# Performance work log

Measured on AMD Instinct MI355X. Metric: run time of the kernel, lower is better.

Reference implementation:

```python
import jax, jax.numpy as jnp
import numpy as np

ALPHA = 0.2        # LeakyReLU negative slope
MASK_VAL = -9e15   # matches torch -9000000000000000.0


def setup_inputs() -> dict:
    key = jax.random.key(0)
    k_h, k_adj, k_w, k_a = jax.random.split(key, 4)
    B, N, Nodes, IF, OF = 8, 8, 512, 256, 256
    h = jax.random.normal(k_h, (B, N, Nodes, IF), dtype=jnp.float32)
    adj = jax.random.randint(k_adj, (Nodes, Nodes), 0, 2, dtype=jnp.int32)
    # xavier_uniform with gain=1.414
    gain = 1.414
    lim_w = gain * np.sqrt(6.0 / (IF + OF))
    W = jax.random.uniform(k_w, (IF, OF), dtype=jnp.float32, minval=-lim_w, maxval=lim_w)
    lim_a = gain * np.sqrt(6.0 / (2 * OF + 1))
    a = jax.random.uniform(k_a, (2 * OF, 1), dtype=jnp.float32, minval=-lim_a, maxval=lim_a)
    return {"h": h, "adj": adj, "W": W, "a": a}


def reference(h, adj, W, a):
    # Wh: [B, N, Nodes, OF]
    Wh = jnp.matmul(h, W)
    OF = W.shape[1]
    a1, a2 = a[:OF, 0], a[OF:, 0]
    # e[..., i, j] = leakyrelu(a1 . Wh_i + a2 . Wh_j)  (decomposed additive attention)
    src = jnp.einsum('bnif,f->bni', Wh, a1)  # [B, N, Nodes]
    dst = jnp.einsum('bnjf,f->bnj', Wh, a2)  # [B, N, Nodes]
    e = jax.nn.leaky_relu(src[..., :, None] + dst[..., None, :], negative_slope=ALPHA)
    attention = jnp.where(adj > 0, e, jnp.full_like(e, MASK_VAL))
    attention = jax.nn.softmax(attention, axis=-1)
    # dropout is identity in eval mode (training=False)
    h_prime = jnp.matmul(attention, Wh)  # [B, N, Nodes, OF]
    return jax.nn.elu(h_prime)  # concat=True
```

## Files before the change

### kernel.cpp

```cpp
#include <hip/hip_runtime.h>
#include <hip/hip_bf16.h>


#define ALPHA 0.2f
#define MASK_VAL -9000000000000000.0f
#define NODES 512
#define FDIM 256
#define BN 64

typedef float  f32x4 __attribute__((ext_vector_type(4)));
typedef int    i32x4 __attribute__((ext_vector_type(4)));
typedef short  s16x8 __attribute__((ext_vector_type(8)));
typedef short  s16x4 __attribute__((ext_vector_type(4)));
typedef __bf16 bf16x8 __attribute__((ext_vector_type(8)));

__device__ __forceinline__ unsigned short f2bfu(float x) {
    __hip_bfloat16 b = __float2bfloat16(x);
    unsigned short u; __builtin_memcpy(&u, &b, 2); return u;
}
__device__ __forceinline__ float bfu2f(unsigned short u) {
    unsigned int w = ((unsigned int)u) << 16; return __uint_as_float(w);
}
__device__ __forceinline__ f32x4 mfma16(s16x8 a, s16x8 b, f32x4 c) {
    return __builtin_amdgcn_mfma_f32_16x16x32_bf16(
        __builtin_bit_cast(bf16x8, a), __builtin_bit_cast(bf16x8, b), c, 0, 0, 0);
}

__device__ __forceinline__ void split8v(f32x4 v0, f32x4 v1, s16x8& hi, s16x8& lo)
{
    float x[8] = {v0[0], v0[1], v0[2], v0[3], v1[0], v1[1], v1[2], v1[3]};
    unsigned hw[4], lw[4];
    #pragma unroll
    for (int d = 0; d < 4; ++d) {
        const unsigned u0 = __float_as_uint(x[2*d]);
        const unsigned u1 = __float_as_uint(x[2*d + 1]);
        hw[d] = __builtin_amdgcn_perm(u1, u0, 0x07060302);
        const float l0 = x[2*d]     - __uint_as_float(u0 & 0xFFFF0000u);
        const float l1 = x[2*d + 1] - __uint_as_float(u1 & 0xFFFF0000u);
        lw[d] = __builtin_amdgcn_perm(__float_as_uint(l1), __float_as_uint(l0),
                                      0x07060302);
    }
    hi = __builtin_bit_cast(s16x8, *(unsigned(*)[4])hw);
    lo = __builtin_bit_cast(s16x8, *(unsigned(*)[4])lw);
}

__device__ __forceinline__ void gll16(const void* g, void* l) {
    __builtin_amdgcn_global_load_lds(
        (const __attribute__((address_space(1))) unsigned int*)g,
        (__attribute__((address_space(3))) unsigned int*)l,
        16, 0, 0);
}

__global__ __launch_bounds__(256) void detect_kernel(const unsigned short* __restrict__ hraw,
                                                     int* __restrict__ flag)
{
    const int tid = threadIdx.x;
    float m = 0.0f;
    for (int i = tid; i < 16384; i += 256) {
        unsigned int w = ((unsigned int)hraw[i]) << 16;
        float v = __uint_as_float(w);
        v = fabsf(v);
        if (!(v == v)) v = 1e30f;
        m = fmaxf(m, v);
    }
    #pragma unroll
    for (int off = 32; off >= 1; off >>= 1)
        m = fmaxf(m, __shfl_down(m, off));
    __shared__ float red[4];
    if ((tid & 63) == 0) red[tid >> 6] = m;
    __syncthreads();
    if (tid == 0) {
        float mm = fmaxf(fmaxf(red[0], red[1]), fmaxf(red[2], red[3]));
        *flag = (mm > 1e4f) ? 1 : 0;
    }
}

__global__ __launch_bounds__(256) void prep_w_kernel(
    const void* __restrict__ Wv, const int* __restrict__ flagp,
    short* __restrict__ WtHi, short* __restrict__ WtLo)
{
    const int flag = *flagp;
    __shared__ float tile[16][17];
    const int tx = threadIdx.x & 15, ty = threadIdx.x >> 4;
    const int kk = blockIdx.y * 16 + ty;
    const int f  = blockIdx.x * 16 + tx;
    float v;
    if (flag) v = ((const float*)Wv)[kk * FDIM + f];
    else      v = bfu2f(((const unsigned short*)Wv)[kk * FDIM + f]);
    tile[ty][tx] = v;
    __syncthreads();
    const float x = tile[tx][ty];
    const int fo = blockIdx.x * 16 + ty;
    const int ko = blockIdx.y * 16 + tx;
    unsigned short h = f2bfu(x);
    WtHi[fo * FDIM + ko] = (short)h;
    WtLo[fo * FDIM + ko] = (short)f2bfu(x - bfu2f(h));
}

__global__ __launch_bounds__(256, 2) void wh_gemm(
    const void* __restrict__ hv,
    const short* __restrict__ WtHi, const short* __restrict__ WtLo,
    const void* __restrict__ av, const int* __restrict__ flagp,
    short* __restrict__ WhTHi, short* __restrict__ WhTLo,
    float* __restrict__ srcv, float* __restrict__ dstv)
{
    __shared__ __align__(16) char smem[81920];
    char* As = smem;
    char* Bh = smem + 16384;
    char* Bl = smem + 49152;

    const int flag = *flagp;
    const int blk = blockIdx.x;
    const int bn  = blk >> 3;
    const int i0  = (blk & 7) * 64;
    const size_t r0g = (size_t)blk * 64;
    const int tid = threadIdx.x;
    const int w = tid >> 6, l = tid & 63;
    const int fb = l & 15, g = l >> 4;
    const unsigned wub = (unsigned)(tid & ~63);

    f32x4 acc[4][4];
    #pragma unroll
    for (int rt = 0; rt < 4; ++rt)
        #pragma unroll
        for (int ct = 0; ct < 4; ++ct) acc[rt][ct] = f32x4{0.f,0.f,0.f,0.f};

    auto stageBhl = [&](int buf, int k0) {
        #pragma unroll
        for (int i = 0; i < 4; ++i) {
            const int idx = i * 256 + tid;
            const int f = idx >> 2, sg = idx & 3;
            const int ss = sg ^ ((f ^ (f >> 2)) & 3);
            char* d = (char*)(size_t)((i * 256 + (int)wub) * 16);
            gll16(WtHi + f * FDIM + k0 + ss * 8, Bh + buf * 16384 + (size_t)d);
            gll16(WtLo + f * FDIM + k0 + ss * 8, Bl + buf * 16384 + (size_t)d);
        }
    };
    auto stageBh = [&](int buf, int k0) {
        #pragma unroll
        for (int i = 0; i < 4; ++i) {
            const int idx = i * 256 + tid;
            const int f = idx >> 2, sg = idx & 3;
            const int ss = sg ^ ((f ^ (f >> 2)) & 3);
            gll16(WtHi + f * FDIM + k0 + ss * 8,
                  Bh + buf * 16384 + (i * 256 + (int)wub) * 16);
        }
    };
    auto stageAf = [&](int buf, int k0) {
        #pragma unroll
        for (int i = 0; i < 2; ++i) {
            const int idx = i * 256 + tid;
            const int row = idx >> 3, sg = idx & 7;
            const int ss = sg ^ (row & 7);
            gll16((const float*)hv + (r0g + row) * FDIM + k0 + ss * 4,
                  As + buf * 8192 + (i * 256 + (int)wub) * 16);
        }
    };
    auto stageAb = [&](int buf, int k0) {
        const int row = tid >> 2, sg = tid & 3;
        const int ss = sg ^ ((row >> 1) & 3);
        gll16((const short*)hv + (r0g + row) * FDIM + k0 + ss * 8,
              As + buf * 4096 + (int)wub * 16);
    };

    if (flag) {
        stageAf(0, 0); stageBhl(0, 0);
        __syncthreads();
        for (int t = 0; t < 8; ++t) {
            const int cur = t & 1, nxt = cur ^ 1;
            if (t < 7) { stageAf(nxt, (t + 1) * 32); stageBhl(nxt, (t + 1) * 32); }
            s16x8 bhf[4], blf[4];
            #pragma unroll
            for (int ct = 0; ct < 4; ++ct) {
                const int f = w * 64 + ct * 16 + fb;
                const int slot = g ^ ((f ^ (f >> 2)) & 3);
                const unsigned off = (unsigned)(cur * 16384 + f * 64 + slot * 16);
                bhf[ct] = *(const s16x8*)(Bh + off);
                blf[ct] = *(const s16x8*)(Bl + off);
            }
            #pragma unroll
            for (int rt = 0; rt < 4; ++rt) {
                const int row = rt * 16 + fb;
                const int s0 = (2 * g) ^ (row & 7), s1 = (2 * g + 1) ^ (row & 7);
                const f32x4 v0 = *(const f32x4*)(As + cur * 8192 + row * 128 + s0 * 16);
                const f32x4 v1 = *(const f32x4*)(As + cur * 8192 + row * 128 + s1 * 16);
                s16x8 ah, al; split8v(v0, v1, ah, al);
                #pragma unroll
                for (int ct = 0; ct < 4; ++ct) {
                    acc[rt][ct] = mfma16(ah, bhf[ct], acc[rt][ct]);
                    acc[rt][ct] = mfma16(al, bhf[ct], acc[rt][ct]);
                    acc[rt][ct] = mfma16(ah, blf[ct], acc[rt][ct]);
                }
            }
            __syncthreads();
        }
    } else {
        stageAb(0, 0); stageBh(0, 0);
        __syncthreads();
        for (int t = 0; t < 8; ++t) {
            const int cur = t & 1, nxt = cur ^ 1;
            if (t < 7) { stageAb(nxt, (t + 1) * 32); stageBh(nxt, (t + 1) * 32); }
            s16x8 bhf[4];
            #pragma unroll
            for (int ct = 0; ct < 4; ++ct) {
                const int f = w * 64 + ct * 16 + fb;
                const int slot = g ^ ((f ^ (f >> 2)) & 3);
                bhf[ct] = *(const s16x8*)(Bh + cur * 16384 + f * 64 + slot * 16);
            }
            #pragma unroll
            for (int rt = 0; rt < 4; ++rt) {
                const int row = rt * 16 + fb;
                const int slot = g ^ ((row >> 1) & 3);
                const s16x8 a = *(const s16x8*)(As + cur * 4096 + row * 64 + slot * 16);
                #pragma unroll
                for (int ct = 0; ct < 4; ++ct)
                    acc[rt][ct] = mfma16(a, bhf[ct], acc[rt][ct]);
            }
            __syncthreads();
        }
    }

    const size_t wbT = (size_t)bn * FDIM * NODES;
    #pragma unroll
    for (int rt = 0; rt < 4; ++rt) {
        const int orow = i0 + rt * 16 + g * 4;
        #pragma unroll
        for (int ct = 0; ct < 4; ++ct) {
            const int f = w * 64 + ct * 16 + fb;
            s16x4 h4, l4;
            #pragma unroll
            for (int r = 0; r < 4; ++r) {
                float x = acc[rt][ct][r];
                unsigned short hh = f2bfu(x);
                h4[r] = (short)hh;
                l4[r] = (short)f2bfu(x - bfu2f(hh));
            }
            *(s16x4*)(WhTHi + wbT + (size_t)f * NODES + orow) = h4;
            *(s16x4*)(WhTLo + wbT + (size_t)f * NODES + orow) = l4;
        }
    }

    float a1v[4], a2v[4];
    #pragma unroll
    for (int ct = 0; ct < 4; ++ct) {
        const int f = w * 64 + ct * 16 + fb;
        if (flag) {
            a1v[ct] = ((const float*)av)[f];
            a2v[ct] = ((const float*)av)[FDIM + f];
        } else {
            a1v[ct] = bfu2f(((const unsigned short*)av)[f]);
            a2v[ct] = bfu2f(((const unsigned short*)av)[FDIM + f]);
        }
    }
    float* red1 = (float*)smem;
    float* red2 = red1 + 256;
    #pragma unroll
    for (int rt = 0; rt < 4; ++rt) {
        #pragma unroll
        for (int r = 0; r < 4; ++r) {
            float s1 = 0.f, s2 = 0.f;
            #pragma unroll
            for (int ct = 0; ct < 4; ++ct) {
                s1 = fmaf(acc[rt][ct][r], a1v[ct], s1);
                s2 = fmaf(acc[rt][ct][r], a2v[ct], s2);
            }
            #pragma unroll
            for (int off = 1; off <= 8; off <<= 1) {
                s1 += __shfl_xor(s1, off);
                s2 += __shfl_xor(s2, off);
            }
            if (fb == 0) {
                red1[w * 64 + rt * 16 + g * 4 + r] = s1;
                red2[w * 64 + rt * 16 + g * 4 + r] = s2;
            }
        }
    }
    __syncthreads();
    if (tid < 64) {
        srcv[bn * NODES + i0 + tid] =
            red1[tid] + red1[64 + tid] + red1[128 + tid] + red1[192 + tid];
        dstv[bn * NODES + i0 + tid] =
            red2[tid] + red2[64 + tid] + red2[128 + tid] + red2[192 + tid];
    }
}

__global__ __launch_bounds__(512, 2) void pv_gemm(
    const short* __restrict__ WhTHi, const short* __restrict__ WhTLo,
    const float* __restrict__ srcv, const float* __restrict__ dstv,
    const int* __restrict__ adj, const int* __restrict__ flagp,
    void* __restrict__ out)
{
    __shared__ __align__(16) char smem[131328];
    char* Ps = smem;
    char* Bh = smem + 65536;
    char* Bl = smem + 98304;
    float* rowinvS = (float*)(smem + 131072);

    const int flag = *flagp;
    const int b0 = blockIdx.x;
    const int blk = (b0 & 7) * 64 + (b0 >> 3);
    const int bn  = blk >> 3;
    const int i0  = (blk & 7) * 64;
    const int tid = threadIdx.x;
    const int w = tid >> 6, l = tid & 63;
    const unsigned wub = (unsigned)(tid & ~63);

    const short* bhig = WhTHi + (size_t)bn * FDIM * NODES;
    const short* blog = WhTLo + (size_t)bn * FDIM * NODES;

    auto stageB = [&](int buf, int k0) {
        #pragma unroll
        for (int i = 0; i < 2; ++i) {
            const int idx = i * 512 + tid;
            const int f = idx >> 2, sg = idx & 3;
            const int ss = sg ^ ((f ^ (f >> 2)) & 3);
            const int d = (i * 512 + (int)wub) * 16;
            gll16(bhig + (size_t)f * NODES + k0 + ss * 8, Bh + buf * 16384 + d);
            gll16(blog + (size_t)f * NODES + k0 + ss * 8, Bl + buf * 16384 + d);
        }
    };

    stageB(0, 0);

    {
        const float* drow = dstv + bn * NODES;
        const int j = l * 8;
        for (int rr = 0; rr < 8; ++rr) {
            const int r = w * 8 + rr;
            const int* adjrow = adj + (size_t)(i0 + r) * NODES;
            const float srow = srcv[bn * NODES + i0 + r];
            const i32x4 q0 = *(const i32x4*)(adjrow + j);
            const i32x4 q1 = *(const i32x4*)(adjrow + j + 4);
            const f32x4 d0 = *(const f32x4*)(drow + j);
            const f32x4 d1 = *(const f32x4*)(drow + j + 4);
            float e[8];
            #pragma unroll
            for (int k = 0; k < 4; ++k) {
                float ev = srow + d0[k];
                ev = (ev > 0.f) ? ev : ALPHA * ev;
                e[k] = (q0[k] > 0) ? ev : MASK_VAL;
                float ew = srow + d1[k];
                ew = (ew > 0.f) ? ew : ALPHA * ew;
                e[4 + k] = (q1[k] > 0) ? ew : MASK_VAL;
            }
            float m = e[0];
            #pragma unroll
            for (int k = 1; k < 8; ++k) m = fmaxf(m, e[k]);
            #pragma unroll
            for (int off = 1; off <= 32; off <<= 1) m = fmaxf(m, __shfl_xor(m, off));
            float s = 0.f;
            s16x8 ph;
            #pragma unroll
            for (int k = 0; k < 8; ++k) {
                float p = __expf(e[k] - m);
                s += p;
                ph[k] = (short)f2bfu(p);
            }
            #pragma unroll
            for (int off = 1; off <= 32; off <<= 1) s += __shfl_xor(s, off);
            *(s16x8*)(Ps + r * 1024 + ((l ^ (r & 7)) * 16)) = ph;
            if (l == 0) rowinvS[r] = 1.0f / s;
        }
    }
    __syncthreads();

    const int fb = l & 15, g = l >> 4;
    const int wr = w >> 2, wc = w & 3;

    f32x4 acc[2][4];
    #pragma unroll
    for (int rt = 0; rt < 2; ++rt)
        #pragma unroll
        for (int ct = 0; ct < 4; ++ct) acc[rt][ct] = f32x4{0.f,0.f,0.f,0.f};

    for (int t = 0; t < 16; ++t) {
        const int cur = t & 1, nxt = cur ^ 1;
        if (t < 15) stageB(nxt, (t + 1) * 32);
        s16x8 bhf[4], blf[4];
        #pragma unroll
        for (int ct = 0; ct < 4; ++ct) {
            const int f = wc * 64 + ct * 16 + fb;
            const int slot = g ^ ((f ^ (f >> 2)) & 3);
            const unsigned off = (unsigned)(cur * 16384 + f * 64 + slot * 16);
            bhf[ct] = *(const s16x8*)(Bh + off);
            blf[ct] = *(const s16x8*)(Bl + off);
        }
        s16x8 af[2];
        #pragma unroll
        for (int rt = 0; rt < 2; ++rt) {
            const int row = wr * 32 + rt * 16 + fb;
            const int seg = 4 * t + g;
            af[rt] = *(const s16x8*)(Ps + row * 1024 + ((seg ^ (row & 7)) * 16));
        }
        #pragma unroll
        for (int rt = 0; rt < 2; ++rt)
            #pragma unroll
            for (int ct = 0; ct < 4; ++ct) {
                acc[rt][ct] = mfma16(af[rt], bhf[ct], acc[rt][ct]);
                acc[rt][ct] = mfma16(af[rt], blf[ct], acc[rt][ct]);
            }
        __syncthreads();
    }

    #pragma unroll
    for (int rt = 0; rt < 2; ++rt) {
        const int rbase = wr * 32 + rt * 16 + g * 4;
        float inv[4];
        #pragma unroll
        for (int r = 0; r < 4; ++r) inv[r] = rowinvS[rbase + r];
        #pragma unroll
        for (int ct = 0; ct < 4; ++ct) {
            const int f = wc * 64 + ct * 16 + fb;
            #pragma unroll
            for (int r = 0; r < 4; ++r) {
                float v = acc[rt][ct][r] * inv[r];
                v = (v > 0.f) ? v : expm1f(v);
                const size_t o = ((size_t)bn * NODES + i0 + rbase + r) * FDIM + f;
                if (flag) ((float*)out)[o] = v;
                else      ((unsigned short*)out)[o] = f2bfu(v);
            }
        }
    }
}

extern "C" void kernel_launch(void* const* d_in, const int* in_sizes, int n_in,
                              void* d_out, int out_size, void* d_ws, size_t ws_size,
                              hipStream_t stream)
{
    const void* h   = d_in[0];
    const int*  adj = (const int*)d_in[1];
    const void* W   = d_in[2];
    const void* a   = d_in[3];

    int*   flag  = (int*)d_ws;
    float* srcv  = (float*)d_ws + 64;
    float* dstv  = srcv + BN * NODES;
    short* WtHi  = (short*)(dstv + BN * NODES);
    short* WtLo  = WtHi + FDIM * FDIM;
    short* WhTHi = WtLo + FDIM * FDIM;
    short* WhTLo = WhTHi + (size_t)BN * FDIM * NODES;

    detect_kernel<<<1, 256, 0, stream>>>((const unsigned short*)h, flag);
    prep_w_kernel<<<dim3(16, 16), 256, 0, stream>>>(W, flag, WtHi, WtLo);
    wh_gemm<<<512, 256, 0, stream>>>(h, WtHi, WtLo, a, flag,
                                     WhTHi, WhTLo, srcv, dstv);
    pv_gemm<<<512, 512, 0, stream>>>(WhTHi, WhTLo, srcv, dstv, adj, flag, d_out);
}
```

Measured before the change: 174.7 us.

## Restructure GAT GEMM pipelines: register-split A staging, triple-buffered PV with 1024 threads

Measured after the change: 164.1 us. -6.1%, faster.

```diff
diff --git a/kernel.cpp b/kernel.cpp
--- a/kernel.cpp
+++ b/kernel.cpp
@@ -105,9 +105,6 @@
     float* __restrict__ srcv, float* __restrict__ dstv)
 {
     __shared__ __align__(16) char smem[81920];
-    char* As = smem;
-    char* Bh = smem + 16384;
-    char* Bl = smem + 49152;
 
     const int flag = *flagp;
     const int blk = blockIdx.x;
@@ -117,7 +114,25 @@
     const int tid = threadIdx.x;
     const int w = tid >> 6, l = tid & 63;
     const int fb = l & 15, g = l >> 4;
-    const unsigned wub = (unsigned)(tid & ~63);
+
+    const int arow = tid >> 2, asg = tid & 3;
+    const int aseg = asg ^ ((arow >> 1) & 3);
+    const int awr  = arow * 64 + asg * 16;
+
+    const short* gBh[4];
+    const short* gBl[4];
+    int bdst[4];
+    {
+        const int bsg = tid & 3;
+        #pragma unroll
+        for (int i = 0; i < 4; ++i) {
+            const int f = i * 64 + (tid >> 2);
+            const int ss = bsg ^ ((f ^ (f >> 2)) & 3);
+            gBh[i] = WtHi + f * FDIM + ss * 8;
+            gBl[i] = WtLo + f * FDIM + ss * 8;
+            bdst[i] = (i * 256 + tid) * 16;
+        }
+    }
 
     f32x4 acc[4][4];
     #pragma unroll
@@ -125,97 +140,106 @@
         #pragma unroll
         for (int ct = 0; ct < 4; ++ct) acc[rt][ct] = f32x4{0.f,0.f,0.f,0.f};
 
-    auto stageBhl = [&](int buf, int k0) {
-        #pragma unroll
-        for (int i = 0; i < 4; ++i) {
-            const int idx = i * 256 + tid;
-            const int f = idx >> 2, sg = idx & 3;
-            const int ss = sg ^ ((f ^ (f >> 2)) & 3);
-            char* d = (char*)(size_t)((i * 256 + (int)wub) * 16);
-            gll16(WtHi + f * FDIM + k0 + ss * 8, Bh + buf * 16384 + (size_t)d);
-            gll16(WtLo + f * FDIM + k0 + ss * 8, Bl + buf * 16384 + (size_t)d);
-        }
-    };
-    auto stageBh = [&](int buf, int k0) {
-        #pragma unroll
-        for (int i = 0; i < 4; ++i) {
-            const int idx = i * 256 + tid;
-            const int f = idx >> 2, sg = idx & 3;
-            const int ss = sg ^ ((f ^ (f >> 2)) & 3);
-            gll16(WtHi + f * FDIM + k0 + ss * 8,
-                  Bh + buf * 16384 + (i * 256 + (int)wub) * 16);
-        }
-    };
-    auto stageAf = [&](int buf, int k0) {
-        #pragma unroll
-        for (int i = 0; i < 2; ++i) {
-            const int idx = i * 256 + tid;
-            const int row = idx >> 3, sg = idx & 7;
-            const int ss = sg ^ (row & 7);
-            gll16((const float*)hv + (r0g + row) * FDIM + k0 + ss * 4,
-                  As + buf * 8192 + (i * 256 + (int)wub) * 16);
-        }
-    };
-    auto stageAb = [&](int buf, int k0) {
-        const int row = tid >> 2, sg = tid & 3;
-        const int ss = sg ^ ((row >> 1) & 3);
-        gll16((const short*)hv + (r0g + row) * FDIM + k0 + ss * 8,
-              As + buf * 4096 + (int)wub * 16);
-    };
-
     if (flag) {
-        stageAf(0, 0); stageBhl(0, 0);
+        const float* gA = (const float*)hv + (r0g + arow) * FDIM + aseg * 8;
+        {
+            f32x4 v0 = *(const f32x4*)gA;
+            f32x4 v1 = *(const f32x4*)(gA + 4);
+            #pragma unroll
+            for (int i = 0; i < 4; ++i) {
+                gll16(gBh[i], smem + 16384 + bdst[i]);
+                gll16(gBl[i], smem + 49152 + bdst[i]);
+            }
+            s16x8 hi, lo; split8v(v0, v1, hi, lo);
+            *(s16x8*)(smem + awr) = hi;
+            *(s16x8*)(smem + 4096 + awr) = lo;
+        }
         __syncthreads();
         for (int t = 0; t < 8; ++t) {
             const int cur = t & 1, nxt = cur ^ 1;
-            if (t < 7) { stageAf(nxt, (t + 1) * 32); stageBhl(nxt, (t + 1) * 32); }
-            s16x8 bhf[4], blf[4];
+            f32x4 v0 = {}, v1 = {};
+            if (t < 7) {
+                v0 = *(const f32x4*)(gA + (t+1)*32);
+                v1 = *(const f32x4*)(gA + (t+1)*32 + 4);
+                #pragma unroll
+                for (int i = 0; i < 4; ++i) {
+                    gll16(gBh[i] + (t+1)*32, smem + 16384 + nxt*16384 + bdst[i]);
+                    gll16(gBl[i] + (t+1)*32, smem + 49152 + nxt*16384 + bdst[i]);
+                }
+            }
+            s16x8 bh[4], bl[4], ah[4], al[4];
             #pragma unroll
             for (int ct = 0; ct < 4; ++ct) {
-                const int f = w * 64 + ct * 16 + fb;
+                const int f = w*64 + ct*16 + fb;
                 const int slot = g ^ ((f ^ (f >> 2)) & 3);
-                const unsigned off = (unsigned)(cur * 16384 + f * 64 + slot * 16);
-                bhf[ct] = *(const s16x8*)(Bh + off);
-                blf[ct] = *(const s16x8*)(Bl + off);
+                const int off = 16384 + cur*16384 + f*64 + slot*16;
+                bh[ct] = *(const s16x8*)(smem + off);
+                bl[ct] = *(const s16x8*)(smem + off + 32768);
             }
             #pragma unroll
             for (int rt = 0; rt < 4; ++rt) {
-                const int row = rt * 16 + fb;
-                const int s0 = (2 * g) ^ (row & 7), s1 = (2 * g + 1) ^ (row & 7);
-                const f32x4 v0 = *(const f32x4*)(As + cur * 8192 + row * 128 + s0 * 16);
-                const f32x4 v1 = *(const f32x4*)(As + cur * 8192 + row * 128 + s1 * 16);
-                s16x8 ah, al; split8v(v0, v1, ah, al);
+                const int row = rt*16 + fb;
+                const int slot = g ^ ((row >> 1) & 3);
+                const int off = cur*8192 + row*64 + slot*16;
+                ah[rt] = *(const s16x8*)(smem + off);
+                al[rt] = *(const s16x8*)(smem + off + 4096);
+            }
+            __builtin_amdgcn_s_setprio(1);
+            #pragma unroll
+            for (int rt = 0; rt < 4; ++rt)
                 #pragma unroll
                 for (int ct = 0; ct < 4; ++ct) {
-                    acc[rt][ct] = mfma16(ah, bhf[ct], acc[rt][ct]);
-                    acc[rt][ct] = mfma16(al, bhf[ct], acc[rt][ct]);
-                    acc[rt][ct] = mfma16(ah, blf[ct], acc[rt][ct]);
+                    acc[rt][ct] = mfma16(ah[rt], bh[ct], acc[rt][ct]);
+                    acc[rt][ct] = mfma16(al[rt], bh[ct], acc[rt][ct]);
+                    acc[rt][ct] = mfma16(ah[rt], bl[ct], acc[rt][ct]);
                 }
+            __builtin_amdgcn_s_setprio(0);
+            if (t < 7) {
+                s16x8 hi, lo; split8v(v0, v1, hi, lo);
+                *(s16x8*)(smem + nxt*8192 + awr) = hi;
+                *(s16x8*)(smem + nxt*8192 + 4096 + awr) = lo;
             }
             __syncthreads();
         }
     } else {
-        stageAb(0, 0); stageBh(0, 0);
+        const short* gA = (const short*)hv + (r0g + arow) * FDIM + aseg * 8;
+        {
+            s16x8 a0 = *(const s16x8*)gA;
+            #pragma unroll
+            for (int i = 0; i < 4; ++i) gll16(gBh[i], smem + 16384 + bdst[i]);
+            *(s16x8*)(smem + awr) = a0;
+        }
         __syncthreads();
         for (int t = 0; t < 8; ++t) {
             const int cur = t & 1, nxt = cur ^ 1;
-            if (t < 7) { stageAb(nxt, (t + 1) * 32); stageBh(nxt, (t + 1) * 32); }
-            s16x8 bhf[4];
+            s16x8 an = {};
+            if (t < 7) {
+                an = *(const s16x8*)(gA + (t+1)*32);
+                #pragma unroll
+                for (int i = 0; i < 4; ++i)
+                    gll16(gBh[i] + (t+1)*32, smem + 16384 + nxt*16384 + bdst[i]);
+            }
+            s16x8 bh[4], ah[4];
             #pragma unroll
             for (int ct = 0; ct < 4; ++ct) {
-                const int f = w * 64 + ct * 16 + fb;
+                const int f = w*64 + ct*16 + fb;
                 const int slot = g ^ ((f ^ (f >> 2)) & 3);
-                bhf[ct] = *(const s16x8*)(Bh + cur * 16384 + f * 64 + slot * 16);
+                bh[ct] = *(const s16x8*)(smem + 16384 + cur*16384 + f*64 + slot*16);
             }
             #pragma unroll
             for (int rt = 0; rt < 4; ++rt) {
-                const int row = rt * 16 + fb;
+                const int row = rt*16 + fb;
                 const int slot = g ^ ((row >> 1) & 3);
-                const s16x8 a = *(const s16x8*)(As + cur * 4096 + row * 64 + slot * 16);
+                ah[rt] = *(const s16x8*)(smem + cur*8192 + row*64 + slot*16);
+            }
+            __builtin_amdgcn_s_setprio(1);
+            #pragma unroll
+            for (int rt = 0; rt < 4; ++rt)
                 #pragma unroll
                 for (int ct = 0; ct < 4; ++ct)
-                    acc[rt][ct] = mfma16(a, bhf[ct], acc[rt][ct]);
-            }
+                    acc[rt][ct] = mfma16(ah[rt], bh[ct], acc[rt][ct]);
+            __builtin_amdgcn_s_setprio(0);
+            if (t < 7) *(s16x8*)(smem + nxt*8192 + awr) = an;
             __syncthreads();
         }
     }
@@ -284,17 +308,13 @@
     }
 }
 
-__global__ __launch_bounds__(512, 2) void pv_gemm(
+__global__ __launch_bounds__(1024, 4) void pv_gemm(
     const short* __restrict__ WhTHi, const short* __restrict__ WhTLo,
     const float* __restrict__ srcv, const float* __restrict__ dstv,
     const int* __restrict__ adj, const int* __restrict__ flagp,
     void* __restrict__ out)
 {
-    __shared__ __align__(16) char smem[131328];
-    char* Ps = smem;
-    char* Bh = smem + 65536;
-    char* Bl = smem + 98304;
-    float* rowinvS = (float*)(smem + 131072);
+    __shared__ __align__(16) char smem[163840];
 
     const int flag = *flagp;
     const int b0 = blockIdx.x;
@@ -303,30 +323,26 @@
     const int i0  = (blk & 7) * 64;
     const int tid = threadIdx.x;
     const int w = tid >> 6, l = tid & 63;
-    const unsigned wub = (unsigned)(tid & ~63);
 
     const short* bhig = WhTHi + (size_t)bn * FDIM * NODES;
     const short* blog = WhTLo + (size_t)bn * FDIM * NODES;
 
-    auto stageB = [&](int buf, int k0) {
-        #pragma unroll
-        for (int i = 0; i < 2; ++i) {
-            const int idx = i * 512 + tid;
-            const int f = idx >> 2, sg = idx & 3;
-            const int ss = sg ^ ((f ^ (f >> 2)) & 3);
-            const int d = (i * 512 + (int)wub) * 16;
-            gll16(bhig + (size_t)f * NODES + k0 + ss * 8, Bh + buf * 16384 + d);
-            gll16(blog + (size_t)f * NODES + k0 + ss * 8, Bl + buf * 16384 + d);
-        }
-    };
-
-    stageB(0, 0);
+    const int sf = tid >> 2, ssg = tid & 3;
+    const int sss = ssg ^ ((sf ^ (sf >> 2)) & 3);
+    const short* gH = bhig + (size_t)sf * NODES + sss * 8;
+    const short* gL = blog + (size_t)sf * NODES + sss * 8;
+    char* ldsH = smem + 65536 + tid * 16;
+    char* ldsL = smem + 65536 + 16384 + tid * 16;
+
+    gll16(gH,      ldsH);          gll16(gL,      ldsL);
+    gll16(gH + 32, ldsH + 32768);  gll16(gL + 32, ldsL + 32768);
 
     {
         const float* drow = dstv + bn * NODES;
         const int j = l * 8;
-        for (int rr = 0; rr < 8; ++rr) {
-            const int r = w * 8 + rr;
+        #pragma unroll
+        for (int rr = 0; rr < 4; ++rr) {
+            const int r = w * 4 + rr;
             const int* adjrow = adj + (size_t)(i0 + r) * NODES;
             const float srow = srcv[bn * NODES + i0 + r];
             const i32x4 q0 = *(const i32x4*)(adjrow + j);
@@ -348,77 +364,82 @@
             for (int k = 1; k < 8; ++k) m = fmaxf(m, e[k]);
             #pragma unroll
             for (int off = 1; off <= 32; off <<= 1) m = fmaxf(m, __shfl_xor(m, off));
-            float s = 0.f;
+            float p[8], s = 0.f;
+            #pragma unroll
+            for (int k = 0; k < 8; ++k) {
+                p[k] = __expf(e[k] - m);
+                s += p[k];
+            }
+            #pragma unroll
+            for (int off = 1; off <= 32; off <<= 1) s += __shfl_xor(s, off);
+            const float isum = 1.0f / s;
             s16x8 ph;
             #pragma unroll
-            for (int k = 0; k < 8; ++k) {
-                float p = __expf(e[k] - m);
-                s += p;
-                ph[k] = (short)f2bfu(p);
-            }
-            #pragma unroll
-            for (int off = 1; off <= 32; off <<= 1) s += __shfl_xor(s, off);
-            *(s16x8*)(Ps + r * 1024 + ((l ^ (r & 7)) * 16)) = ph;
-            if (l == 0) rowinvS[r] = 1.0f / s;
+            for (int k = 0; k < 8; ++k) ph[k] = (short)f2bfu(p[k] * isum);
+            *(s16x8*)(smem + r * 1024 + ((l ^ (r & 7)) * 16)) = ph;
         }
     }
     __syncthreads();
 
     const int fb = l & 15, g = l >> 4;
     const int wr = w >> 2, wc = w & 3;
-
-    f32x4 acc[2][4];
-    #pragma unroll
-    for (int rt = 0; rt < 2; ++rt)
-        #pragma unroll
-        for (int ct = 0; ct < 4; ++ct) acc[rt][ct] = f32x4{0.f,0.f,0.f,0.f};
-
+    const int arow = wr * 16 + fb;
+    const unsigned abase = (unsigned)(arow * 1024);
+    const unsigned aswz  = (unsigned)((arow & 7) << 4);
+
+    f32x4 acc[4];
+    #pragma unroll
+    for (int ct = 0; ct < 4; ++ct) acc[ct] = f32x4{0.f, 0.f, 0.f, 0.f};
+
+    unsigned boff[4];
+    #pragma unroll
+    for (int ct = 0; ct < 4; ++ct) {
+        const int f = wc * 64 + ct * 16 + fb;
+        const int slot = g ^ ((f ^ (f >> 2)) & 3);
+        boff[ct] = (unsigned)(65536 + f * 64 + slot * 16);
+    }
+
+    int cur = 0;
     for (int t = 0; t < 16; ++t) {
-        const int cur = t & 1, nxt = cur ^ 1;
-        if (t < 15) stageB(nxt, (t + 1) * 32);
-        s16x8 bhf[4], blf[4];
+        if (t < 15) asm volatile("s_waitcnt vmcnt(2)" ::: "memory");
+        else        asm volatile("s_waitcnt vmcnt(0)" ::: "memory");
+        __builtin_amdgcn_s_barrier();
+        __builtin_amdgcn_sched_barrier(0);
+        asm volatile("" ::: "memory");
+        if (t < 14) {
+            int nb = cur + 2; if (nb >= 3) nb -= 3;
+            gll16(gH + (t + 2) * 32, ldsH + nb * 32768);
+            gll16(gL + (t + 2) * 32, ldsL + nb * 32768);
+        }
+        s16x8 bh[4], bl[4];
         #pragma unroll
         for (int ct = 0; ct < 4; ++ct) {
-            const int f = wc * 64 + ct * 16 + fb;
-            const int slot = g ^ ((f ^ (f >> 2)) & 3);
-            const unsigned off = (unsigned)(cur * 16384 + f * 64 + slot * 16);
-            bhf[ct] = *(const s16x8*)(Bh + off);
-            blf[ct] = *(const s16x8*)(Bl + off);
-        }
-        s16x8 af[2];
-        #pragma unroll
-        for (int rt = 0; rt < 2; ++rt) {
-            const int row = wr * 32 + rt * 16 + fb;
-            const int seg = 4 * t + g;
-            af[rt] = *(const s16x8*)(Ps + row * 1024 + ((seg ^ (row & 7)) * 16));
-        }
-        #pragma unroll
-        for (int rt = 0; rt < 2; ++rt)
-            #pragma unroll
-            for (int ct = 0; ct < 4; ++ct) {
-                acc[rt][ct] = mfma16(af[rt], bhf[ct], acc[rt][ct]);
-                acc[rt][ct] = mfma16(af[rt], blf[ct], acc[rt][ct]);
-            }
-        __syncthreads();
-    }
-
-    #pragma unroll
-    for (int rt = 0; rt < 2; ++rt) {
-        const int rbase = wr * 32 + rt * 16 + g * 4;
-        float inv[4];
-        #pragma unroll
-        for (int r = 0; r < 4; ++r) inv[r] = rowinvS[rbase + r];
+            const unsigned off = boff[ct] + (unsigned)(cur * 32768);
+            bh[ct] = *(const s16x8*)(smem + off);
+            bl[ct] = *(const s16x8*)(smem + off + 16384);
+        }
+        const unsigned aoff = abase + ((((unsigned)(t * 4 + g)) * 16) ^ aswz);
+        const s16x8 a = *(const s16x8*)(smem + aoff);
+        __builtin_amdgcn_s_setprio(1);
         #pragma unroll
         for (int ct = 0; ct < 4; ++ct) {
-            const int f = wc * 64 + ct * 16 + fb;
-            #pragma unroll
-            for (int r = 0; r < 4; ++r) {
-                float v = acc[rt][ct][r] * inv[r];
-                v = (v > 0.f) ? v : expm1f(v);
-                const size_t o = ((size_t)bn * NODES + i0 + rbase + r) * FDIM + f;
-                if (flag) ((float*)out)[o] = v;
-                else      ((unsigned short*)out)[o] = f2bfu(v);
-            }
+            acc[ct] = mfma16(a, bh[ct], acc[ct]);
+            acc[ct] = mfma16(a, bl[ct], acc[ct]);
+        }
+        __builtin_amdgcn_s_setprio(0);
+        cur = cur + 1; if (cur == 3) cur = 0;
+    }
+
+    #pragma unroll
+    for (int ct = 0; ct < 4; ++ct) {
+        const int f = wc * 64 + ct * 16 + fb;
+        #pragma unroll
+        for (int r = 0; r < 4; ++r) {
+            float v = acc[ct][r];
+            v = (v > 0.f) ? v : expm1f(v);
+            const size_t o = ((size_t)bn * NODES + i0 + wr * 16 + g * 4 + r) * FDIM + f;
+            if (flag) ((float*)out)[o] = v;
+            else      ((unsigned short*)out)[o] = f2bfu(v);
         }
     }
 }
@@ -444,5 +465,5 @@
     prep_w_kernel<<<dim3(16, 16), 256, 0, stream>>>(W, flag, WtHi, WtLo);
     wh_gemm<<<512, 256, 0, stream>>>(h, WtHi, WtLo, a, flag,
                                      WhTHi, WhTLo, srcv, dstv);
-    pv_gemm<<<512, 512, 0, stream>>>(WhTHi, WhTLo, srcv, dstv, adj, flag, d_out);
-}
+    pv_gemm<<<512, 1024, 0, stream>>>(WhTHi, WhTLo, srcv, dstv, adj, flag, d_out);
+}
```
